# Kernel optimization log

Hardware: AMD Instinct MI355X
Metric: run time of the kernel (lower is better)

## Reference

```python
import jax, jax.numpy as jnp
import numpy as np

B, C, H, W = 8, 256, 128, 128


def setup_inputs() -> dict:
    key = jax.random.key(0)
    ks = jax.random.split(key, 8)
    s = 1.0 / np.sqrt(C)
    return {
        "edge_feature": jax.random.normal(ks[0], (B, C, H, W), jnp.float32),
        "mask_feature": jax.random.normal(ks[1], (B, C, H, W), jnp.float32),
        # 1x1 conv weights [out_dim, in_dim] + biases
        "Wq": jax.random.normal(ks[2], (C, C), jnp.float32) * s,
        "bq": jax.random.normal(ks[3], (C,), jnp.float32) * 0.01,
        "Wk": jax.random.normal(ks[4], (C, C), jnp.float32) * s,
        "bk": jax.random.normal(ks[5], (C,), jnp.float32) * 0.01,
        "Wv": jax.random.normal(ks[6], (C, C), jnp.float32) * s,
        "bv": jax.random.normal(ks[7], (C,), jnp.float32) * 0.01,
        # torch initializes gamma=0; use 0.5 so the attention path is exercised
        "gamma": jnp.array(0.5, jnp.float32),
    }


def _conv1x1(x, w, b):
    # x: [B,C,H,W], w: [O,C] -> [B,O,H,W]
    return jnp.einsum('oc,bchw->bohw', w, x) + b[None, :, None, None]


def reference(edge_feature, mask_feature, Wq, bq, Wk, bk, Wv, bv, gamma):
    b, c, h, w = edge_feature.shape
    q = _conv1x1(edge_feature, Wq, bq)
    k = _conv1x1(edge_feature, Wk, bk)
    v = _conv1x1(mask_feature, Wv, bv)

    # Criss-cross energies (note: source forward does NOT apply the INF diag mask)
    energy_H = jnp.einsum('bchw,bcjw->bhwj', q, k)  # [B,H,W,H] column attention
    energy_W = jnp.einsum('bchw,bchj->bhwj', q, k)  # [B,H,W,W] row attention

    att = jax.nn.softmax(jnp.concatenate([energy_H, energy_W], axis=3), axis=3)
    att_H4 = att[..., :h]   # [B,H,W,H]
    att_W4 = att[..., h:]   # [B,H,W,W]

    out_H = jnp.einsum('bcjw,bhwj->bchw', v, att_H4)
    out_W = jnp.einsum('bchj,bhwj->bchw', v, att_W4)
    out = gamma * (out_H + out_W) + mask_feature

    # Match torch's returned attention layouts: [B*W,H,H] and [B*H,W,W]
    att_H = jnp.transpose(att_H4, (0, 2, 1, 3)).reshape(b * w, h, h)
    att_W = att_W4.reshape(b * h, w, w)
    return (out, att_H, att_W)
```

## Files before the change

### kernel.cpp

```cpp
#include <hip/hip_runtime.h>

typedef unsigned short u16;
typedef unsigned int   u32;
typedef __attribute__((ext_vector_type(8))) short short8;
typedef __attribute__((ext_vector_type(4))) float f32x4;

#define HW_   16384
constexpr long CHW_ = 4194304L;
constexpr long NT   = 33554432L;

#define GLDS(g, l) __builtin_amdgcn_global_load_lds( \
    (const __attribute__((address_space(1))) void*)(g), \
    (__attribute__((address_space(3))) void*)(l), 16, 0, 0)

__device__ inline u16 f2bf(float x){ u32 u = __float_as_uint(x); u += 0x7fff + ((u>>16)&1); return (u16)(u>>16); }
__device__ inline float bf2f(u16 h){ return __uint_as_float(((u32)h)<<16); }

__device__ inline void wait_vm(int n){
  if (n >= 8)       asm volatile("s_waitcnt vmcnt(8)"  ::: "memory");
  else if (n == 4)  asm volatile("s_waitcnt vmcnt(4)"  ::: "memory");
  else              asm volatile("s_waitcnt vmcnt(0)"  ::: "memory");
}

__device__ inline const short8* frg(const u16* T, int r, int c){
  return (const short8*)(T + r*64 + ((c ^ (r&7))<<3));
}

template<int MODE, bool SPLIT>
__global__ __launch_bounds__(256) void gemm_nt(
    const u16* __restrict__ Ah, const u16* __restrict__ Al,
    const u16* __restrict__ Bh, const u16* __restrict__ Bl,
    const float* __restrict__ bias, const float* __restrict__ gammap,
    float* __restrict__ outF, u16* __restrict__ outH, u16* __restrict__ outL,
    u16* __restrict__ outH2, u16* __restrict__ outL2, int dirH)
{
  constexpr int K    = (MODE == 3) ? 128 : 256;
  constexpr int NTl  = K / 32;
  constexpr int BUFU = SPLIT ? 16384 : 8192;
  constexpr int GPS  = SPLIT ? 8 : 4;
  __shared__ __align__(16) u16 smem[2][BUFU];

  const int t    = threadIdx.x;
  const int lane = t & 63;
  const int wid  = t >> 6;
  const int wr   = (wid >> 1) << 6;
  const int wc   = (wid & 1) << 6;

  long abase, bbase, ars, brs;
  int b = 0, m0 = 0, n0 = 0, xx = 0, s = 0, ct = 0;

  if constexpr (MODE == 0) {
    b = blockIdx.z; m0 = blockIdx.x << 7; n0 = blockIdx.y << 7;
    abase = ((long)b * HW_ + m0) * 256; ars = 256;
    bbase = (long)n0 * 256;             brs = 256;
  } else if constexpr (MODE == 1) {
    s = blockIdx.x; b = s >> 7; xx = s & 127;
    abase = dirH ? ((long)b * HW_ + xx) * 256 : ((long)b * HW_ + (long)xx * 128) * 256;
    ars   = dirH ? 32768 : 256;
    bbase = abase; brs = ars;
  } else if constexpr (MODE == 2) {
    b = blockIdx.z; m0 = blockIdx.y << 7; n0 = blockIdx.x << 7;
    abase = (long)m0 * 256;             ars = 256;
    bbase = ((long)b * HW_ + n0) * 256; brs = 256;
  } else {
    s = blockIdx.x; ct = blockIdx.y; b = s >> 7; xx = s & 127;
    abase = ((long)b * 256 + (long)(ct << 7)) * HW_ + (long)xx * 128; ars = HW_;
    bbase = (long)s * HW_; brs = 128;
  }

  const u16* pA0 = Ah + abase;
  const u16* pA1 = SPLIT ? (Al + abase) : (Bh + bbase);
  const long rsA1 = SPLIT ? ars : brs;
  const u16* pB0 = SPLIT ? (Bh + bbase) : nullptr;
  const u16* pB1 = SPLIT ? (Bl + bbase) : nullptr;

  f32x4 acc[4][4];
  for (int i = 0; i < 4; i++)
    for (int j = 0; j < 4; j++)
      acc[i][j] = (f32x4){0.f, 0.f, 0.f, 0.f};

  auto stage = [&](int buf, int step) {
    const long ko = (long)step * 32;
    u16* T1b = &smem[buf][0];
    #pragma unroll
    for (int i = 0; i < 4; i++) {
      int r = (i << 5) + (t >> 3);
      int c = (t & 7) ^ (r & 7);
      const u16* g = (c < 4 ? pA0 + (long)r * ars : pA1 + (long)r * rsA1) + ko + ((c & 3) << 3);
      GLDS(g, T1b + (i << 11) + ((t >> 6) << 9));
    }
    if constexpr (SPLIT) {
      u16* T2b = &smem[buf][8192];
      #pragma unroll
      for (int i = 0; i < 4; i++) {
        int r = (i << 5) + (t >> 3);
        int c = (t & 7) ^ (r & 7);
        const u16* g = (c < 4 ? pB0 + (long)r * brs : pB1 + (long)r * brs) + ko + ((c & 3) << 3);
        GLDS(g, T2b + (i << 11) + ((t >> 6) << 9));
      }
    }
  };

  const int khi = lane >> 4;
  const int rl  = lane & 15;

  stage(0, 0);
  stage(1, 1);

  #pragma unroll
  for (int kt = 0; kt < NTl; ++kt) {
    wait_vm((kt + 1 < NTl ? 1 : 0) * GPS);
    __builtin_amdgcn_sched_barrier(0);
    __builtin_amdgcn_s_barrier();
    __builtin_amdgcn_sched_barrier(0);

    const u16* T1 = &smem[kt & 1][0];
    const u16* T2 = SPLIT ? &smem[kt & 1][8192] : &smem[kt & 1][0];

    short8 ah[4], al[4], bh[4], bl[4];
    #pragma unroll
    for (int f = 0; f < 4; f++) {
      ah[f] = *frg(T1, wr + f * 16 + rl, khi);
      if constexpr (SPLIT) {
        al[f] = *frg(T1, wr + f * 16 + rl, 4 + khi);
        bh[f] = *frg(T2, wc + f * 16 + rl, khi);
        bl[f] = *frg(T2, wc + f * 16 + rl, 4 + khi);
      } else {
        bh[f] = *frg(T1, wc + f * 16 + rl, 4 + khi);
      }
    }

    __builtin_amdgcn_s_setprio(1);
    #pragma unroll
    for (int fm = 0; fm < 4; fm++) {
      #pragma unroll
      for (int fn = 0; fn < 4; fn++) {
        acc[fm][fn] = __builtin_amdgcn_mfma_f32_16x16x32_bf16(ah[fm], bh[fn], acc[fm][fn], 0, 0, 0);
        if constexpr (SPLIT) {
          acc[fm][fn] = __builtin_amdgcn_mfma_f32_16x16x32_bf16(ah[fm], bl[fn], acc[fm][fn], 0, 0, 0);
          acc[fm][fn] = __builtin_amdgcn_mfma_f32_16x16x32_bf16(al[fm], bh[fn], acc[fm][fn], 0, 0, 0);
        }
      }
    }
    __builtin_amdgcn_s_setprio(0);

    __builtin_amdgcn_s_barrier();
    __builtin_amdgcn_sched_barrier(0);
    if (kt + 2 < NTl) stage(kt & 1, kt + 2);
  }

  float gma = 0.f;
  if constexpr (MODE == 3) gma = gammap[0];

  #pragma unroll
  for (int fm = 0; fm < 4; fm++) {
    #pragma unroll
    for (int fn = 0; fn < 4; fn++) {
      #pragma unroll
      for (int r = 0; r < 4; r++) {
        int lr = wr + fm * 16 + ((lane >> 4) << 2) + r;
        int lc = wc + fn * 16 + (lane & 15);
        float v = acc[fm][fn][r];
        if constexpr (MODE == 0) {
          float v2 = v + bias[n0 + lc];
          int col = (n0 + lc) & 255;
          long idx = ((long)b * HW_ + m0 + lr) * 256 + col;
          u16 h = f2bf(v2);
          u16 l = f2bf(v2 - bf2f(h));
          if (n0 < 256) { outH[idx] = h; outL[idx] = l; }
          else          { outH2[idx] = h; outL2[idx] = l; }
        } else if constexpr (MODE == 1) {
          outF[(long)s * HW_ + (long)lr * 128 + lc] = v;
        } else if constexpr (MODE == 2) {
          v += bias[m0 + lr];
          outH[((long)b * 256 + m0 + lr) * HW_ + n0 + lc] = f2bf(v);
        } else {
          long off = ((long)b * 256 + (long)(ct << 7) + lr) * HW_ + (long)xx * 128 + lc;
          outH[off] = f2bf(gma * v);
        }
      }
    }
  }
}

__global__ __launch_bounds__(256) void split_transpose2(const float* __restrict__ edge,
    const float* __restrict__ mask, u16* __restrict__ hi, u16* __restrict__ lo,
    u16* __restrict__ mt)
{
  int b = blockIdx.z, c0 = blockIdx.y << 5, p0 = blockIdx.x << 5;
  __shared__ float tileE[32][33];
  __shared__ float tileM[32][33];
  int tx = threadIdx.x, ty = threadIdx.y;
  const float* E = edge + (long)b * CHW_;
  const float* M = mask + (long)b * CHW_;
  #pragma unroll
  for (int r = 0; r < 4; r++) {
    int cc = ty + (r << 3);
    long g = (long)(c0 + cc) * HW_ + p0 + tx;
    tileE[cc][tx] = E[g];
    tileM[cc][tx] = M[g];
  }
  __syncthreads();
  #pragma unroll
  for (int r = 0; r < 4; r++) {
    int pp = ty + (r << 3);
    long idx = ((long)b * HW_ + p0 + pp) * 256 + c0 + tx;
    float x = tileE[tx][pp];
    u16 h = f2bf(x);
    hi[idx] = h;
    lo[idx] = f2bf(x - bf2f(h));
    mt[idx] = f2bf(tileM[tx][pp]);
  }
}

__global__ __launch_bounds__(256) void wsplit(const float* __restrict__ Wq,
    const float* __restrict__ Wk, const float* __restrict__ Wv,
    const float* __restrict__ bq, const float* __restrict__ bk,
    u16* cath, u16* catl, u16* vh, float* bcat)
{
  int i = blockIdx.x * 256 + threadIdx.x;
  float q = Wq[i]; u16 a = f2bf(q); cath[i] = a; catl[i] = f2bf(q - bf2f(a));
  float k = Wk[i]; u16 c = f2bf(k); cath[65536 + i] = c; catl[65536 + i] = f2bf(k - bf2f(c));
  vh[i] = f2bf(Wv[i]);
  if (blockIdx.x == 0) {
    bcat[threadIdx.x]       = bq[threadIdx.x];
    bcat[256 + threadIdx.x] = bk[threadIdx.x];
  }
}

__global__ __launch_bounds__(256) void transpose_hw_bf16(const u16* __restrict__ src,
                                                         u16* __restrict__ dst)
{
  int bc = blockIdx.z;
  int h0 = blockIdx.x << 5, w0 = blockIdx.y << 5;
  long base = (long)bc * HW_;
  __shared__ u16 tile[32][34];
  int tx = threadIdx.x, ty = threadIdx.y;
  #pragma unroll
  for (int r = 0; r < 4; r++)
    tile[ty + (r << 3)][tx] = src[base + (long)(h0 + ty + (r << 3)) * 128 + w0 + tx];
  __syncthreads();
  #pragma unroll
  for (int r = 0; r < 4; r++) {
    int ww = ty + (r << 3);
    dst[base + (long)(w0 + ww) * 128 + h0 + tx] = tile[tx][ww];
  }
}

__global__ __launch_bounds__(256) void softmax_kernel(float* __restrict__ attH,
    float* __restrict__ attW, u16* __restrict__ aHb, u16* __restrict__ aWb)
{
  int wid  = threadIdx.x >> 6;
  int lane = threadIdx.x & 63;
  long r = (long)blockIdx.x * 4 + wid;
  int b = (int)(r >> 14);
  int h = (int)((r >> 7) & 127);
  int w = (int)(r & 127);
  long baseH = ((long)(b * 128 + w) * 128 + h) * 128;
  long baseW = r * 128;
  float* rowH = attH + baseH;
  float* rowW = attW + baseW;
  float x0 = rowH[lane], x1 = rowH[64 + lane], x2 = rowW[lane], x3 = rowW[64 + lane];
  float m = fmaxf(fmaxf(x0, x1), fmaxf(x2, x3));
  #pragma unroll
  for (int off = 32; off; off >>= 1) m = fmaxf(m, __shfl_xor(m, off, 64));
  float e0 = expf(x0 - m), e1 = expf(x1 - m), e2 = expf(x2 - m), e3 = expf(x3 - m);
  float ssum = e0 + e1 + e2 + e3;
  #pragma unroll
  for (int off = 32; off; off >>= 1) ssum += __shfl_xor(ssum, off, 64);
  float inv = 1.0f / ssum;
  float p0 = e0 * inv, p1 = e1 * inv, p2 = e2 * inv, p3 = e3 * inv;
  rowH[lane] = p0; rowH[64 + lane] = p1;
  rowW[lane] = p2; rowW[64 + lane] = p3;
  aHb[baseH + lane] = f2bf(p0); aHb[baseH + 64 + lane] = f2bf(p1);
  aWb[baseW + lane] = f2bf(p2); aWb[baseW + 64 + lane] = f2bf(p3);
}

__global__ __launch_bounds__(256) void merge_kernel(const u16* __restrict__ tmp,
    const u16* __restrict__ pW, const float* __restrict__ mask, float* __restrict__ out)
{
  int bc = blockIdx.z;
  int h0 = blockIdx.x << 5, w0 = blockIdx.y << 5;
  long base = (long)bc * HW_;
  __shared__ u16 tile[32][33];
  int tx = threadIdx.x, ty = threadIdx.y;
  #pragma unroll
  for (int r = 0; r < 4; r++) {
    int ww = ty + (r << 3);
    tile[ww][tx] = tmp[base + (long)(w0 + ww) * 128 + h0 + tx];
  }
  __syncthreads();
  #pragma unroll
  for (int r = 0; r < 4; r++) {
    int hh = ty + (r << 3);
    long o = base + (long)(h0 + hh) * 128 + w0 + tx;
    out[o] = bf2f(pW[o]) + bf2f(tile[tx][hh]) + mask[o];
  }
}

extern "C" void kernel_launch(void* const* d_in, const int* in_sizes, int n_in,
                              void* d_out, int out_size, void* d_ws, size_t ws_size,
                              hipStream_t stream) {
  const float* edge  = (const float*)d_in[0];
  const float* mask  = (const float*)d_in[1];
  const float* Wq    = (const float*)d_in[2];
  const float* bq    = (const float*)d_in[3];
  const float* Wk    = (const float*)d_in[4];
  const float* bk    = (const float*)d_in[5];
  const float* Wv    = (const float*)d_in[6];
  const float* bv    = (const float*)d_in[7];
  const float* gamma = (const float*)d_in[8];

  float* out  = (float*)d_out;
  float* attH = out + NT;
  float* attW = attH + 16777216L;

  char* W = (char*)d_ws;
  const long SLOT = 67108864L;
  u16* Xth = (u16*)(W + 0 * SLOT);
  u16* Xtl = (u16*)(W + 1 * SLOT);
  u16* Mt  = (u16*)(W + 2 * SLOT);
  u16* Qh  = (u16*)(W + 3 * SLOT);
  u16* Ql  = (u16*)(W + 4 * SLOT);
  u16* Kh  = (u16*)(W + 5 * SLOT);
  u16* Kl  = (u16*)(W + 6 * SLOT);
  u16* Vb  = (u16*)(W + 7 * SLOT);
  u16* Vtb = (u16*)(W + 0 * SLOT);
  u16* aWb = (u16*)(W + 1 * SLOT);
  u16* aHb = (u16*)(W + 1 * SLOT + 33554432L);
  u16* tmp = (u16*)(W + 3 * SLOT);
  u16* pW  = (u16*)(W + 4 * SLOT);
  u16* Wch = (u16*)(W + 8 * SLOT);
  u16* Wcl = Wch + 131072;
  u16* Wvh = Wcl + 131072;
  float* bcat = (float*)(Wvh + 65536);

  dim3 tb(32, 8);

  wsplit<<<256, 256, 0, stream>>>(Wq, Wk, Wv, bq, bk, Wch, Wcl, Wvh, bcat);
  split_transpose2<<<dim3(512, 8, 8), tb, 0, stream>>>(edge, mask, Xth, Xtl, Mt);

  gemm_nt<0, true><<<dim3(128, 4, 8), 256, 0, stream>>>(
      Xth, Xtl, Wch, Wcl, bcat, nullptr, nullptr, Qh, Ql, Kh, Kl, 0);
  gemm_nt<2, false><<<dim3(128, 2, 8), 256, 0, stream>>>(
      Wvh, nullptr, Mt, nullptr, bv, nullptr, nullptr, Vb, nullptr, nullptr, nullptr, 0);

  transpose_hw_bf16<<<dim3(4, 4, 2048), tb, 0, stream>>>(Vb, Vtb);

  gemm_nt<1, true><<<dim3(1024), 256, 0, stream>>>(
      Qh, Ql, Kh, Kl, nullptr, nullptr, attW, nullptr, nullptr, nullptr, nullptr, 0);
  gemm_nt<1, true><<<dim3(1024), 256, 0, stream>>>(
      Qh, Ql, Kh, Kl, nullptr, nullptr, attH, nullptr, nullptr, nullptr, nullptr, 1);

  softmax_kernel<<<dim3(32768), 256, 0, stream>>>(attH, attW, aHb, aWb);

  gemm_nt<3, false><<<dim3(1024, 2), 256, 0, stream>>>(
      Vtb, nullptr, aHb, nullptr, nullptr, gamma, nullptr, tmp, nullptr, nullptr, nullptr, 0);
  gemm_nt<3, false><<<dim3(1024, 2), 256, 0, stream>>>(
      Vb, nullptr, aWb, nullptr, nullptr, gamma, nullptr, pW, nullptr, nullptr, nullptr, 0);

  merge_kernel<<<dim3(4, 4, 2048), tb, 0, stream>>>(tmp, pW, mask, out);
}
```

Before: 745.9 us.

## Interleave hi/lo bf16 splits per K-block and stage epilogues through LDS

Stores the hi and lo bf16 halves of X, W, Q and K interleaved in 32-element blocks within each row. Each stage then issues one contiguous load per operand, and the GEMM template drops the separate split pointers. Every GEMM epilogue now writes the accumulator tile to LDS and then emits vectorized 16-byte row-contiguous stores instead of scattered scalar stores. The two attention-energy launches are merged into one grid, and softmax is rewritten to use 32-lane groups with vector loads and stores. The costs are extra LDS traffic and a block-wide sync in the epilogue, plus a more complex indexing scheme that must match across kernels.

```diff
diff --git a/kernel.cpp b/kernel.cpp
--- a/kernel.cpp
+++ b/kernel.cpp
@@ -16,29 +16,20 @@
 __device__ inline u16 f2bf(float x){ u32 u = __float_as_uint(x); u += 0x7fff + ((u>>16)&1); return (u16)(u>>16); }
 __device__ inline float bf2f(u16 h){ return __uint_as_float(((u32)h)<<16); }
 
-__device__ inline void wait_vm(int n){
-  if (n >= 8)       asm volatile("s_waitcnt vmcnt(8)"  ::: "memory");
-  else if (n == 4)  asm volatile("s_waitcnt vmcnt(4)"  ::: "memory");
-  else              asm volatile("s_waitcnt vmcnt(0)"  ::: "memory");
-}
-
 __device__ inline const short8* frg(const u16* T, int r, int c){
   return (const short8*)(T + r*64 + ((c ^ (r&7))<<3));
 }
 
-template<int MODE, bool SPLIT>
+
+template<int MODE>
 __global__ __launch_bounds__(256) void gemm_nt(
-    const u16* __restrict__ Ah, const u16* __restrict__ Al,
-    const u16* __restrict__ Bh, const u16* __restrict__ Bl,
+    const char* __restrict__ Aq, const char* __restrict__ Bq,
     const float* __restrict__ bias, const float* __restrict__ gammap,
-    float* __restrict__ outF, u16* __restrict__ outH, u16* __restrict__ outL,
-    u16* __restrict__ outH2, u16* __restrict__ outL2, int dirH)
-{
-  constexpr int K    = (MODE == 3) ? 128 : 256;
-  constexpr int NTl  = K / 32;
-  constexpr int BUFU = SPLIT ? 16384 : 8192;
-  constexpr int GPS  = SPLIT ? 8 : 4;
-  __shared__ __align__(16) u16 smem[2][BUFU];
+    float* __restrict__ outFa, float* __restrict__ outFb,
+    u16* __restrict__ outUa, u16* __restrict__ outUb)
+{
+  constexpr int NTl = (MODE <= 1) ? 8 : (MODE == 2 ? 4 : 2);
+  __shared__ __align__(16) u16 smem[34048];
 
   const int t    = threadIdx.x;
   const int lane = t & 63;
@@ -46,58 +37,49 @@
   const int wr   = (wid >> 1) << 6;
   const int wc   = (wid & 1) << 6;
 
-  long abase, bbase, ars, brs;
-  int b = 0, m0 = 0, n0 = 0, xx = 0, s = 0, ct = 0;
+  long abase = 0, bbase = 0, ars = 0, brs = 0;
+  int b = 0, m0 = 0, n0 = 0, xx = 0, ct = 0, dir = 0, sOut = 0;
 
   if constexpr (MODE == 0) {
     b = blockIdx.z; m0 = blockIdx.x << 7; n0 = blockIdx.y << 7;
-    abase = ((long)b * HW_ + m0) * 256; ars = 256;
-    bbase = (long)n0 * 256;             brs = 256;
+    abase = ((long)b * HW_ + m0) * 1024; ars = 1024;
+    bbase = (long)n0 * 1024;             brs = 1024;
   } else if constexpr (MODE == 1) {
-    s = blockIdx.x; b = s >> 7; xx = s & 127;
-    abase = dirH ? ((long)b * HW_ + xx) * 256 : ((long)b * HW_ + (long)xx * 128) * 256;
-    ars   = dirH ? 32768 : 256;
+    int bid = blockIdx.x;
+    b = bid >> 8; dir = (bid >> 7) & 1; xx = bid & 127;
+    sOut = b * 128 + xx;
+    if (dir) { abase = (long)b * 16777216L + (long)xx * 1024; ars = 131072; }
+    else     { abase = (long)b * 16777216L + (long)xx * 131072; ars = 1024; }
     bbase = abase; brs = ars;
   } else if constexpr (MODE == 2) {
     b = blockIdx.z; m0 = blockIdx.y << 7; n0 = blockIdx.x << 7;
-    abase = (long)m0 * 256;             ars = 256;
-    bbase = ((long)b * HW_ + n0) * 256; brs = 256;
+    abase = (long)m0 * 512;              ars = 512;
+    bbase = ((long)b * HW_ + n0) * 512;  brs = 512;
   } else {
-    s = blockIdx.x; ct = blockIdx.y; b = s >> 7; xx = s & 127;
-    abase = ((long)b * 256 + (long)(ct << 7)) * HW_ + (long)xx * 128; ars = HW_;
-    bbase = (long)s * HW_; brs = 128;
-  }
-
-  const u16* pA0 = Ah + abase;
-  const u16* pA1 = SPLIT ? (Al + abase) : (Bh + bbase);
-  const long rsA1 = SPLIT ? ars : brs;
-  const u16* pB0 = SPLIT ? (Bh + bbase) : nullptr;
-  const u16* pB1 = SPLIT ? (Bl + bbase) : nullptr;
+    int s = blockIdx.x; ct = blockIdx.y; b = s >> 7; xx = s & 127;
+    sOut = s;
+    abase = ((long)b * 256 + (long)(ct << 7)) * 32768L + (long)xx * 256; ars = 32768;
+    bbase = (long)s * 32768L; brs = 256;
+  }
+
+  const char* pA = Aq + abase;
+  const char* pB = Bq + bbase;
 
   f32x4 acc[4][4];
   for (int i = 0; i < 4; i++)
     for (int j = 0; j < 4; j++)
       acc[i][j] = (f32x4){0.f, 0.f, 0.f, 0.f};
 
-  auto stage = [&](int buf, int step) {
-    const long ko = (long)step * 32;
-    u16* T1b = &smem[buf][0];
+  auto stage = [&](int buf, int kt) {
+    u16* T1 = smem + buf * 17024;
+    u16* T2 = T1 + 8192;
+    const long ko = (long)kt * 128;
     #pragma unroll
     for (int i = 0; i < 4; i++) {
       int r = (i << 5) + (t >> 3);
       int c = (t & 7) ^ (r & 7);
-      const u16* g = (c < 4 ? pA0 + (long)r * ars : pA1 + (long)r * rsA1) + ko + ((c & 3) << 3);
-      GLDS(g, T1b + (i << 11) + ((t >> 6) << 9));
-    }
-    if constexpr (SPLIT) {
-      u16* T2b = &smem[buf][8192];
-      #pragma unroll
-      for (int i = 0; i < 4; i++) {
-        int r = (i << 5) + (t >> 3);
-        int c = (t & 7) ^ (r & 7);
-        const u16* g = (c < 4 ? pB0 + (long)r * brs : pB1 + (long)r * brs) + ko + ((c & 3) << 3);
-        GLDS(g, T2b + (i << 11) + ((t >> 6) << 9));
-      }
+      GLDS(pA + (long)r * ars + ko + (c << 4), T1 + (i << 11) + ((t >> 6) << 9));
+      GLDS(pB + (long)r * brs + ko + (c << 4), T2 + (i << 11) + ((t >> 6) << 9));
     }
   };
 
@@ -109,25 +91,22 @@
 
   #pragma unroll
   for (int kt = 0; kt < NTl; ++kt) {
-    wait_vm((kt + 1 < NTl ? 1 : 0) * GPS);
+    if (kt + 1 < NTl) asm volatile("s_waitcnt vmcnt(8)" ::: "memory");
+    else              asm volatile("s_waitcnt vmcnt(0)" ::: "memory");
     __builtin_amdgcn_sched_barrier(0);
     __builtin_amdgcn_s_barrier();
     __builtin_amdgcn_sched_barrier(0);
 
-    const u16* T1 = &smem[kt & 1][0];
-    const u16* T2 = SPLIT ? &smem[kt & 1][8192] : &smem[kt & 1][0];
-
-    short8 ah[4], al[4], bh[4], bl[4];
+    const u16* T1 = smem + (kt & 1) * 17024;
+    const u16* T2 = T1 + 8192;
+
+    short8 fa0[4], fa1[4], fb0[4], fb1[4];
     #pragma unroll
     for (int f = 0; f < 4; f++) {
-      ah[f] = *frg(T1, wr + f * 16 + rl, khi);
-      if constexpr (SPLIT) {
-        al[f] = *frg(T1, wr + f * 16 + rl, 4 + khi);
-        bh[f] = *frg(T2, wc + f * 16 + rl, khi);
-        bl[f] = *frg(T2, wc + f * 16 + rl, 4 + khi);
-      } else {
-        bh[f] = *frg(T1, wc + f * 16 + rl, 4 + khi);
-      }
+      fa0[f] = *frg(T1, wr + f * 16 + rl, khi);
+      fa1[f] = *frg(T1, wr + f * 16 + rl, 4 + khi);
+      fb0[f] = *frg(T2, wc + f * 16 + rl, khi);
+      fb1[f] = *frg(T2, wc + f * 16 + rl, 4 + khi);
     }
 
     __builtin_amdgcn_s_setprio(1);
@@ -135,10 +114,13 @@
     for (int fm = 0; fm < 4; fm++) {
       #pragma unroll
       for (int fn = 0; fn < 4; fn++) {
-        acc[fm][fn] = __builtin_amdgcn_mfma_f32_16x16x32_bf16(ah[fm], bh[fn], acc[fm][fn], 0, 0, 0);
-        if constexpr (SPLIT) {
-          acc[fm][fn] = __builtin_amdgcn_mfma_f32_16x16x32_bf16(ah[fm], bl[fn], acc[fm][fn], 0, 0, 0);
-          acc[fm][fn] = __builtin_amdgcn_mfma_f32_16x16x32_bf16(al[fm], bh[fn], acc[fm][fn], 0, 0, 0);
+        if constexpr (MODE <= 1) {
+          acc[fm][fn] = __builtin_amdgcn_mfma_f32_16x16x32_bf16(fa0[fm], fb0[fn], acc[fm][fn], 0, 0, 0);
+          acc[fm][fn] = __builtin_amdgcn_mfma_f32_16x16x32_bf16(fa0[fm], fb1[fn], acc[fm][fn], 0, 0, 0);
+          acc[fm][fn] = __builtin_amdgcn_mfma_f32_16x16x32_bf16(fa1[fm], fb0[fn], acc[fm][fn], 0, 0, 0);
+        } else {
+          acc[fm][fn] = __builtin_amdgcn_mfma_f32_16x16x32_bf16(fa0[fm], fb0[fn], acc[fm][fn], 0, 0, 0);
+          acc[fm][fn] = __builtin_amdgcn_mfma_f32_16x16x32_bf16(fa1[fm], fb1[fn], acc[fm][fn], 0, 0, 0);
         }
       }
     }
@@ -151,6 +133,7 @@
 
   float gma = 0.f;
   if constexpr (MODE == 3) gma = gammap[0];
+  float* LDSE = (float*)smem;
 
   #pragma unroll
   for (int fm = 0; fm < 4; fm++) {
@@ -159,33 +142,67 @@
       #pragma unroll
       for (int r = 0; r < 4; r++) {
         int lr = wr + fm * 16 + ((lane >> 4) << 2) + r;
-        int lc = wc + fn * 16 + (lane & 15);
+        int lc = wc + fn * 16 + rl;
         float v = acc[fm][fn][r];
-        if constexpr (MODE == 0) {
-          float v2 = v + bias[n0 + lc];
-          int col = (n0 + lc) & 255;
-          long idx = ((long)b * HW_ + m0 + lr) * 256 + col;
-          u16 h = f2bf(v2);
-          u16 l = f2bf(v2 - bf2f(h));
-          if (n0 < 256) { outH[idx] = h; outL[idx] = l; }
-          else          { outH2[idx] = h; outL2[idx] = l; }
-        } else if constexpr (MODE == 1) {
-          outF[(long)s * HW_ + (long)lr * 128 + lc] = v;
-        } else if constexpr (MODE == 2) {
-          v += bias[m0 + lr];
-          outH[((long)b * 256 + m0 + lr) * HW_ + n0 + lc] = f2bf(v);
-        } else {
-          long off = ((long)b * 256 + (long)(ct << 7) + lr) * HW_ + (long)xx * 128 + lc;
-          outH[off] = f2bf(gma * v);
-        }
+        if constexpr (MODE == 0) v += bias[n0 + lc];
+        if constexpr (MODE == 2) v += bias[m0 + lr];
+        if constexpr (MODE == 3) v *= gma;
+        LDSE[lr * 132 + lc] = v;
       }
     }
   }
+  __syncthreads();
+
+  if constexpr (MODE == 0) {
+    u16* outp = (n0 < 256) ? outUa : outUb;
+    long rowb = ((long)b * HW_ + m0) * 512;
+    int cbu = (n0 & 255) * 2;
+    #pragma unroll
+    for (int k = 0; k < 16; ++k) {
+      int row = k * 8 + (t >> 5);
+      int iu  = (t & 31) * 8;
+      int off = iu & 63;
+      int lcol = (iu >> 6) * 32 + (off & 31);
+      const float* src = &LDSE[row * 132 + lcol];
+      u16 o[8];
+      if (off < 32) {
+        #pragma unroll
+        for (int j = 0; j < 8; j++) o[j] = f2bf(src[j]);
+      } else {
+        #pragma unroll
+        for (int j = 0; j < 8; j++) { float v = src[j]; u16 h = f2bf(v); o[j] = f2bf(v - bf2f(h)); }
+      }
+      *(short8*)(outp + rowb + (long)row * 512 + cbu + iu) = *(short8*)o;
+    }
+  } else if constexpr (MODE == 1) {
+    float* op = dir ? outFb : outFa;
+    long ob = (long)sOut * 16384;
+    #pragma unroll
+    for (int k = 0; k < 16; ++k) {
+      int row = k * 8 + (t >> 5);
+      int c4 = (t & 31) * 4;
+      f32x4 v = *(const f32x4*)&LDSE[row * 132 + c4];
+      *(f32x4*)(op + ob + (long)row * 128 + c4) = v;
+    }
+  } else {
+    #pragma unroll
+    for (int k = 0; k < 8; ++k) {
+      int row = k * 16 + (t >> 4);
+      int c8 = (t & 15) * 8;
+      const float* src = &LDSE[row * 132 + c8];
+      u16 o[8];
+      #pragma unroll
+      for (int j = 0; j < 8; j++) o[j] = f2bf(src[j]);
+      long addr;
+      if constexpr (MODE == 2) addr = ((long)b * 256 + m0 + row) * HW_ + n0 + c8;
+      else                     addr = ((long)b * 256 + (ct << 7) + row) * HW_ + (long)xx * 128 + c8;
+      *(short8*)(outUa + addr) = *(short8*)o;
+    }
+  }
 }
 
 __global__ __launch_bounds__(256) void split_transpose2(const float* __restrict__ edge,
-    const float* __restrict__ mask, u16* __restrict__ hi, u16* __restrict__ lo,
-    u16* __restrict__ mt)
+    const float* __restrict__ mask, u16* __restrict__ Xs, u16* __restrict__ Mt)
 {
   int b = blockIdx.z, c0 = blockIdx.y << 5, p0 = blockIdx.x << 5;
   __shared__ float tileE[32][33];
@@ -201,27 +218,31 @@
     tileM[cc][tx] = M[g];
   }
   __syncthreads();
+  int blk = (c0 >> 5) * 64;
   #pragma unroll
   for (int r = 0; r < 4; r++) {
     int pp = ty + (r << 3);
-    long idx = ((long)b * HW_ + p0 + pp) * 256 + c0 + tx;
+    long prow = (long)b * HW_ + p0 + pp;
     float x = tileE[tx][pp];
     u16 h = f2bf(x);
-    hi[idx] = h;
-    lo[idx] = f2bf(x - bf2f(h));
-    mt[idx] = f2bf(tileM[tx][pp]);
+    Xs[prow * 512 + blk + tx]      = h;
+    Xs[prow * 512 + blk + 32 + tx] = f2bf(x - bf2f(h));
+    Mt[prow * 256 + c0 + tx]       = f2bf(tileM[tx][pp]);
   }
 }
 
 __global__ __launch_bounds__(256) void wsplit(const float* __restrict__ Wq,
     const float* __restrict__ Wk, const float* __restrict__ Wv,
     const float* __restrict__ bq, const float* __restrict__ bk,
-    u16* cath, u16* catl, u16* vh, float* bcat)
+    u16* Wc, u16* Wvp, float* bcat)
 {
   int i = blockIdx.x * 256 + threadIdx.x;
-  float q = Wq[i]; u16 a = f2bf(q); cath[i] = a; catl[i] = f2bf(q - bf2f(a));
-  float k = Wk[i]; u16 c = f2bf(k); cath[65536 + i] = c; catl[65536 + i] = f2bf(k - bf2f(c));
-  vh[i] = f2bf(Wv[i]);
+  int o = i >> 8, c = i & 255;
+  long pos = (long)o * 512 + (c >> 5) * 64 + (c & 31);
+  float q = Wq[i]; u16 a = f2bf(q); Wc[pos] = a; Wc[pos + 32] = f2bf(q - bf2f(a));
+  float k = Wk[i]; u16 d = f2bf(k);
+  Wc[pos + 131072] = d; Wc[pos + 131072 + 32] = f2bf(k - bf2f(d));
+  Wvp[i] = f2bf(Wv[i]);
   if (blockIdx.x == 0) {
     bcat[threadIdx.x]       = bq[threadIdx.x];
     bcat[256 + threadIdx.x] = bk[threadIdx.x];
@@ -250,30 +271,37 @@
 __global__ __launch_bounds__(256) void softmax_kernel(float* __restrict__ attH,
     float* __restrict__ attW, u16* __restrict__ aHb, u16* __restrict__ aWb)
 {
-  int wid  = threadIdx.x >> 6;
-  int lane = threadIdx.x & 63;
-  long r = (long)blockIdx.x * 4 + wid;
+  int g  = threadIdx.x & 31;
+  long r = (long)blockIdx.x * 8 + (threadIdx.x >> 5);
   int b = (int)(r >> 14);
   int h = (int)((r >> 7) & 127);
   int w = (int)(r & 127);
   long baseH = ((long)(b * 128 + w) * 128 + h) * 128;
   long baseW = r * 128;
-  float* rowH = attH + baseH;
-  float* rowW = attW + baseW;
-  float x0 = rowH[lane], x1 = rowH[64 + lane], x2 = rowW[lane], x3 = rowW[64 + lane];
-  float m = fmaxf(fmaxf(x0, x1), fmaxf(x2, x3));
-  #pragma unroll
-  for (int off = 32; off; off >>= 1) m = fmaxf(m, __shfl_xor(m, off, 64));
-  float e0 = expf(x0 - m), e1 = expf(x1 - m), e2 = expf(x2 - m), e3 = expf(x3 - m);
-  float ssum = e0 + e1 + e2 + e3;
-  #pragma unroll
-  for (int off = 32; off; off >>= 1) ssum += __shfl_xor(ssum, off, 64);
-  float inv = 1.0f / ssum;
-  float p0 = e0 * inv, p1 = e1 * inv, p2 = e2 * inv, p3 = e3 * inv;
-  rowH[lane] = p0; rowH[64 + lane] = p1;
-  rowW[lane] = p2; rowW[64 + lane] = p3;
-  aHb[baseH + lane] = f2bf(p0); aHb[baseH + 64 + lane] = f2bf(p1);
-  aWb[baseW + lane] = f2bf(p2); aWb[baseW + 64 + lane] = f2bf(p3);
+  float* rp = (g < 16) ? (attH + baseH) : (attW + baseW);
+  u16*   up = (g < 16) ? (aHb + baseH)  : (aWb + baseW);
+  int j0 = (g & 15) * 8;
+  f32x4 v0 = *(f32x4*)(rp + j0);
+  f32x4 v1 = *(f32x4*)(rp + j0 + 4);
+  float m = fmaxf(fmaxf(fmaxf(v0.x, v0.y), fmaxf(v0.z, v0.w)),
+                  fmaxf(fmaxf(v1.x, v1.y), fmaxf(v1.z, v1.w)));
+  #pragma unroll
+  for (int off = 16; off; off >>= 1) m = fmaxf(m, __shfl_xor(m, off, 32));
+  float e[8];
+  e[0]=expf(v0.x-m); e[1]=expf(v0.y-m); e[2]=expf(v0.z-m); e[3]=expf(v0.w-m);
+  e[4]=expf(v1.x-m); e[5]=expf(v1.y-m); e[6]=expf(v1.z-m); e[7]=expf(v1.w-m);
+  float s = ((e[0]+e[1])+(e[2]+e[3])) + ((e[4]+e[5])+(e[6]+e[7]));
+  #pragma unroll
+  for (int off = 16; off; off >>= 1) s += __shfl_xor(s, off, 32);
+  float inv = 1.0f / s;
+  #pragma unroll
+  for (int j = 0; j < 8; j++) e[j] *= inv;
+  *(f32x4*)(rp + j0)     = (f32x4){e[0], e[1], e[2], e[3]};
+  *(f32x4*)(rp + j0 + 4) = (f32x4){e[4], e[5], e[6], e[7]};
+  u16 o[8];
+  #pragma unroll
+  for (int j = 0; j < 8; j++) o[j] = f2bf(e[j]);
+  *(short8*)(up + j0) = *(short8*)o;
 }
 
 __global__ __launch_bounds__(256) void merge_kernel(const u16* __restrict__ tmp,
@@ -316,48 +344,41 @@
   float* attW = attH + 16777216L;
 
   char* W = (char*)d_ws;
-  const long SLOT = 67108864L;
-  u16* Xth = (u16*)(W + 0 * SLOT);
-  u16* Xtl = (u16*)(W + 1 * SLOT);
-  u16* Mt  = (u16*)(W + 2 * SLOT);
-  u16* Qh  = (u16*)(W + 3 * SLOT);
-  u16* Ql  = (u16*)(W + 4 * SLOT);
-  u16* Kh  = (u16*)(W + 5 * SLOT);
-  u16* Kl  = (u16*)(W + 6 * SLOT);
-  u16* Vb  = (u16*)(W + 7 * SLOT);
-  u16* Vtb = (u16*)(W + 0 * SLOT);
-  u16* aWb = (u16*)(W + 1 * SLOT);
-  u16* aHb = (u16*)(W + 1 * SLOT + 33554432L);
-  u16* tmp = (u16*)(W + 3 * SLOT);
-  u16* pW  = (u16*)(W + 4 * SLOT);
-  u16* Wch = (u16*)(W + 8 * SLOT);
-  u16* Wcl = Wch + 131072;
-  u16* Wvh = Wcl + 131072;
-  float* bcat = (float*)(Wvh + 65536);
+  u16* Xs  = (u16*)(W);
+  u16* Mt  = (u16*)(W + 134217728L);
+  u16* Qs  = (u16*)(W + 201326592L);
+  u16* Ks  = (u16*)(W + 335544320L);
+  u16* Vb  = (u16*)(W + 469762048L);
+  u16* Wc  = (u16*)(W + 536870912L);
+  u16* Wvp = Wc + 262144;
+  float* bcat = (float*)(Wvp + 65536);
+  u16* Vtb = (u16*)(W);
+  u16* aWb = (u16*)(W + 67108864L);
+  u16* aHb = (u16*)(W + 100663296L);
+  u16* tmp = (u16*)(W + 201326592L);
+  u16* pW  = (u16*)(W + 335544320L);
 
   dim3 tb(32, 8);
 
-  wsplit<<<256, 256, 0, stream>>>(Wq, Wk, Wv, bq, bk, Wch, Wcl, Wvh, bcat);
-  split_transpose2<<<dim3(512, 8, 8), tb, 0, stream>>>(edge, mask, Xth, Xtl, Mt);
-
-  gemm_nt<0, true><<<dim3(128, 4, 8), 256, 0, stream>>>(
-      Xth, Xtl, Wch, Wcl, bcat, nullptr, nullptr, Qh, Ql, Kh, Kl, 0);
-  gemm_nt<2, false><<<dim3(128, 2, 8), 256, 0, stream>>>(
-      Wvh, nullptr, Mt, nullptr, bv, nullptr, nullptr, Vb, nullptr, nullptr, nullptr, 0);
+  wsplit<<<256, 256, 0, stream>>>(Wq, Wk, Wv, bq, bk, Wc, Wvp, bcat);
+  split_transpose2<<<dim3(512, 8, 8), tb, 0, stream>>>(edge, mask, Xs, Mt);
+
+  gemm_nt<0><<<dim3(128, 4, 8), 256, 0, stream>>>(
+      (const char*)Xs, (const char*)Wc, bcat, nullptr, nullptr, nullptr, Qs, Ks);
+  gemm_nt<2><<<dim3(128, 2, 8), 256, 0, stream>>>(
+      (const char*)Wvp, (const char*)Mt, bv, nullptr, nullptr, nullptr, Vb, nullptr);
 
   transpose_hw_bf16<<<dim3(4, 4, 2048), tb, 0, stream>>>(Vb, Vtb);
 
-  gemm_nt<1, true><<<dim3(1024), 256, 0, stream>>>(
-      Qh, Ql, Kh, Kl, nullptr, nullptr, attW, nullptr, nullptr, nullptr, nullptr, 0);
-  gemm_nt<1, true><<<dim3(1024), 256, 0, stream>>>(
-      Qh, Ql, Kh, Kl, nullptr, nullptr, attH, nullptr, nullptr, nullptr, nullptr, 1);
-
-  softmax_kernel<<<dim3(32768), 256, 0, stream>>>(attH, attW, aHb, aWb);
-
-  gemm_nt<3, false><<<dim3(1024, 2), 256, 0, stream>>>(
-      Vtb, nullptr, aHb, nullptr, nullptr, gamma, nullptr, tmp, nullptr, nullptr, nullptr, 0);
-  gemm_nt<3, false><<<dim3(1024, 2), 256, 0, stream>>>(
-      Vb, nullptr, aWb, nullptr, nullptr, gamma, nullptr, pW, nullptr, nullptr, nullptr, 0);
+  gemm_nt<1><<<dim3(2048), 256, 0, stream>>>(
+      (const char*)Qs, (const char*)Ks, nullptr, nullptr, attW, attH, nullptr, nullptr);
+
+  softmax_kernel<<<dim3(16384), 256, 0, stream>>>(attH, attW, aHb, aWb);
+
+  gemm_nt<3><<<dim3(1024, 2), 256, 0, stream>>>(
+      (const char*)Vtb, (const char*)aHb, nullptr, gamma, nullptr, nullptr, tmp, nullptr);
+  gemm_nt<3><<<dim3(1024, 2), 256, 0, stream>>>(
+      (const char*)Vb, (const char*)aWb, nullptr, gamma, nullptr, nullptr, pW, nullptr);
 
   merge_kernel<<<dim3(4, 4, 2048), tb, 0, stream>>>(tmp, pW, mask, out);
 }
```

Result: faster. 634.3 us (-15.0%).
